# Kernel optimization log

Measured on AMD Instinct MI355X. Metric: run time of the kernel, lower is better.

The kernel has to match this reference:

```python
import math
import jax, jax.numpy as jnp
import numpy as np

B, L, H = 32, 1024, 128

def setup_inputs() -> dict:
    key = jax.random.key(0)
    k1, k2, k3, k4 = jax.random.split(key, 4)
    a = jax.random.normal(k1, (B, L, H), dtype=jnp.float32)
    b = jax.random.normal(k2, (B, L, H), dtype=jnp.float32)
    mask_a = jax.random.randint(k3, (B, L, 1), 0, 2, dtype=jnp.int32)
    mask_b = jax.random.randint(k4, (B, L, 1), 0, 2, dtype=jnp.int32)
    temperature = jnp.asarray(1.0 / math.sqrt(H), dtype=jnp.float32)
    return {"a": a, "b": b, "mask_a": mask_a, "mask_b": mask_b, "temperature": temperature}

def reference(a, b, mask_a, mask_b, temperature):
    # scores: [B, La, Lb]
    scores = jnp.einsum('bld,bmd->blm', a, b) * temperature
    # outer product of token validity masks -> pair mask [B, La, Lb]
    mask = jnp.einsum('blk,bmk->blm', mask_a.astype(jnp.float32), mask_b.astype(jnp.float32)) > 0
    scores = jnp.where(mask, scores, jnp.float32(-10000.0))
    attention_a = jax.nn.softmax(scores, axis=1)  # normalize over La (columns)
    attention_b = jax.nn.softmax(scores, axis=2)  # normalize over Lb (rows)
    feature_a = jnp.einsum('blm,bmd->bld', attention_b, b)
    feature_b = jnp.einsum('blm,bmd->bld', attention_a, a)  # valid since La == Lb
    return (feature_a, feature_b)
```

## Files before the change

kernel.cpp:

```cpp
#include <hip/hip_runtime.h>
#include <math.h>

#define BN 32
#define LL 1024
#define HH 128

typedef __attribute__((ext_vector_type(8))) short short8;
typedef __attribute__((ext_vector_type(4))) float f32x4;

static const size_t SZ_BF = (size_t)BN * LL * HH * 2;

__device__ __forceinline__ ushort f2bf(float x) {
  union { float f; unsigned u; } c; c.f = x;
  unsigned r = c.u + 0x7fffu + ((c.u >> 16) & 1u);
  return (ushort)(r >> 16);
}
__device__ __forceinline__ float bf2f(ushort h) {
  union { unsigned u; float f; } c; c.u = ((unsigned)h) << 16;
  return c.f;
}
__device__ __forceinline__ short8 ld8(const ushort* p) {
  return *(const short8*)p;
}

__global__ __launch_bounds__(256) void k_convert(
    const float* __restrict__ a, const float* __restrict__ b,
    const int* __restrict__ mask_b,
    ushort* __restrict__ abf, ushort* __restrict__ bbf,
    ushort* __restrict__ aT, ushort* __restrict__ bT,
    float* __restrict__ meanb, float* __restrict__ invmean) {
  int bb = blockIdx.y;
  int l0 = blockIdx.x * 64;
  int which = blockIdx.z;
  const float* src = which ? b : a;
  ushort* dst  = which ? bbf : abf;
  ushort* dstT = which ? bT : aT;
  float* dmean = which ? meanb : invmean;
  __shared__ __align__(16) ushort T[128][72];
  __shared__ float accS[128];
  __shared__ float wgt[64];
  int t = threadIdx.x;
  if (t < 128) accS[t] = 0.f;
  if (t < 64)
    wgt[t] = which ? 1.0f : ((mask_b[bb * LL + l0 + t] == 0) ? 1.0f : 0.0f);
  int lrow = t >> 5;
  int dcol = (t & 31) * 4;
#pragma unroll
  for (int p = 0; p < 8; ++p) {
    int l = p * 8 + lrow;
    float4 v = *(const float4*)&src[((size_t)bb * LL + l0 + l) * HH + dcol];
    ushort4 u;
    u.x = f2bf(v.x); u.y = f2bf(v.y); u.z = f2bf(v.z); u.w = f2bf(v.w);
    *(ushort4*)&dst[((size_t)bb * LL + l0 + l) * HH + dcol] = u;
    T[dcol + 0][l] = u.x; T[dcol + 1][l] = u.y;
    T[dcol + 2][l] = u.z; T[dcol + 3][l] = u.w;
  }
  __syncthreads();
  int drow = t >> 3;
  int c8 = (t & 7) * 8;
#pragma unroll
  for (int q = 0; q < 4; ++q) {
    int d = q * 32 + drow;
    short8 val = *(const short8*)&T[d][c8];
    *(short8*)&dstT[((size_t)bb * HH + d) * LL + l0 + c8] = val;
    float s = 0.f;
#pragma unroll
    for (int j = 0; j < 8; ++j) s += wgt[c8 + j] * bf2f((ushort)val[j]);
    atomicAdd(&accS[d], s);
  }
  __syncthreads();
  if (t < 128) atomicAdd(&dmean[bb * HH + t], accS[t]);
}


__global__ __launch_bounds__(256, 2) void k_colsum(
    const ushort* __restrict__ abf, const ushort* __restrict__ bbf,
    const int* __restrict__ mask_a, const int* __restrict__ mask_b,
    const float* __restrict__ temp_p, float2* __restrict__ cc) {
  int wg = blockIdx.x;
  int xcd = wg & 7, k_ = wg >> 3;
  int bb = (k_ >> 4) * 8 + xcd;
  int m0 = (k_ & 15) * 64;
  int t = threadIdx.x;
  int w = t >> 6, lane = t & 63, l16 = lane & 15, quad = lane >> 4;
  float temp = temp_p[0];
  __shared__ __align__(16) float biasA[LL];
  __shared__ float csred[4][4][16];
  for (int i = t; i < LL; i += 256)
    biasA[i] = mask_a[bb * LL + i] ? 0.0f : -10000.0f;

  short8 Bm[4][4];
  float biasB_mt[4];
#pragma unroll
  for (int mt = 0; mt < 4; ++mt) {
    int m = m0 + mt * 16 + l16;
    biasB_mt[mt] = mask_b[bb * LL + m] ? 0.0f : -10000.0f;
#pragma unroll
    for (int k = 0; k < 4; ++k)
      Bm[mt][k] = ld8(&bbf[((size_t)bb * LL + m) * HH + k * 32 + quad * 8]);
  }
  __syncthreads();

  float cs[4] = {0.f, 0.f, 0.f, 0.f};
  short8 Al0[4], Al1[4];

#define LOADAL(AlX, IT)                                                       \
  {                                                                           \
    const ushort* arow = &abf[((size_t)bb * LL + w * 256 + (IT) * 16 + l16) * HH]; \
    _Pragma("unroll") for (int k = 0; k < 4; ++k)                             \
        AlX[k] = ld8(&arow[k * 32 + quad * 8]);                               \
  }

#define CSCOMPUTE(AlX, IT)                                                    \
  {                                                                           \
    int lbase = w * 256 + (IT) * 16;                                          \
    f32x4 bA = *(const f32x4*)&biasA[lbase + quad * 4];                       \
    _Pragma("unroll") for (int mt = 0; mt < 4; ++mt) {                        \
      f32x4 sacc = {0.f, 0.f, 0.f, 0.f};                                      \
      _Pragma("unroll") for (int k = 0; k < 4; ++k)                           \
          sacc = __builtin_amdgcn_mfma_f32_16x16x32_bf16(AlX[k], Bm[mt][k],   \
                                                         sacc, 0, 0, 0);      \
      _Pragma("unroll") for (int r = 0; r < 4; ++r)                           \
          cs[mt] += __expf(sacc[r] * temp + bA[r] + biasB_mt[mt]);            \
    }                                                                         \
  }

  LOADAL(Al0, 0);
  for (int it = 0; it < 16; it += 2) {
    LOADAL(Al1, it + 1);
    CSCOMPUTE(Al0, it);
    LOADAL(Al0, (it + 2) & 15);
    CSCOMPUTE(Al1, it + 1);
  }
#undef LOADAL
#undef CSCOMPUTE

#pragma unroll
  for (int mt = 0; mt < 4; ++mt) {
    cs[mt] += __shfl_xor(cs[mt], 16);
    cs[mt] += __shfl_xor(cs[mt], 32);
  }
  if (lane < 16) {
#pragma unroll
    for (int mt = 0; mt < 4; ++mt) csred[w][mt][l16] = cs[mt];
  }
  __syncthreads();
  if (t < 64) {
    int mt = t >> 4, ml = t & 15;
    float s = csred[0][mt][ml] + csred[1][mt][ml] + csred[2][mt][ml] + csred[3][mt][ml];
    int m = m0 + t;
    float bB = mask_b[bb * LL + m] ? 0.0f : -10000.0f;
    cc[bb * LL + m] = make_float2(s > 0.f ? 1.0f / s : 0.0f, bB);
  }
}

__global__ __launch_bounds__(256, 2) void k_features(
    const ushort* __restrict__ abf, const ushort* __restrict__ bbf,
    const ushort* __restrict__ aT, const ushort* __restrict__ bT,
    const int* __restrict__ mask_a, const float* __restrict__ temp_p,
    const float2* __restrict__ cc, const float* __restrict__ meanb,
    const float* __restrict__ invmean, float* __restrict__ out) {
  int wg = blockIdx.x;
  int xcd = wg & 7, k_ = wg >> 3;
  int bb = (k_ >> 4) * 8 + xcd;
  int l0 = (k_ & 15) * 64;
  int t = threadIdx.x;
  int w = t >> 6, lane = t & 63, l16 = lane & 15, quad = lane >> 4;
  float temp = temp_p[0];

  __shared__ float2 ccs[LL];
  __shared__ __align__(16) ushort Pa[2][64 * 72];
  __shared__ __align__(16) ushort Pb[2][64 * 72];
  __shared__ float rspart[4][64];
  __shared__ float rsfin[64];

  for (int i = t; i < LL; i += 256) ccs[i] = cc[bb * LL + i];

  float biasA_lt[4];
  short8 Afix[4][4];
#pragma unroll
  for (int lt = 0; lt < 4; ++lt) {
    int l = l0 + lt * 16 + l16;
    biasA_lt[lt] = mask_a[bb * LL + l] ? 0.0f : -10000.0f;
#pragma unroll
    for (int k = 0; k < 4; ++k)
      Afix[lt][k] = ld8(&abf[((size_t)bb * LL + l) * HH + k * 32 + quad * 8]);
  }

  f32x4 accA[4][2], accB[4][2];
  f32x4 zero = {0.f, 0.f, 0.f, 0.f};
#pragma unroll
  for (int lt = 0; lt < 4; ++lt)
#pragma unroll
    for (int dt = 0; dt < 2; ++dt) { accA[lt][dt] = zero; accB[lt][dt] = zero; }
  float rs_lt[4] = {0.f, 0.f, 0.f, 0.f};
  __syncthreads();

  short8 Am0[4], Am1[4];
  float2 cv0[4], cv1[4];
  short8 Bb[2][2], Ba[2][2];

#define LOADAM(AmX, cvX, M0)                                                  \
  {                                                                           \
    const ushort* brow = &bbf[((size_t)bb * LL + (M0) + w * 16 + l16) * HH];  \
    _Pragma("unroll") for (int k = 0; k < 4; ++k)                             \
        AmX[k] = ld8(&brow[k * 32 + quad * 8]);                               \
    _Pragma("unroll") for (int r = 0; r < 4; ++r)                             \
        cvX[r] = ccs[(M0) + w * 16 + quad * 4 + r];                           \
  }

#define LOADBT(M0)                                                            \
  {                                                                           \
    _Pragma("unroll") for (int dt = 0; dt < 2; ++dt) {                        \
      const ushort* btrow =                                                   \
          &bT[((size_t)bb * HH + w * 32 + dt * 16 + l16) * LL + (M0)];        \
      const ushort* atrow =                                                   \
          &aT[((size_t)bb * HH + w * 32 + dt * 16 + l16) * LL + (M0)];        \
      _Pragma("unroll") for (int ks = 0; ks < 2; ++ks) {                      \
        Bb[dt][ks] = ld8(&btrow[ks * 32 + quad * 8]);                         \
        Ba[dt][ks] = ld8(&atrow[ks * 32 + quad * 8]);                         \
      }                                                                       \
    }                                                                         \
  }

#define SPHASE(AmX, cvX)                                                      \
  {                                                                           \
    ushort* pa = &Pa[buf][0];                                                 \
    ushort* pb = &Pb[buf][0];                                                 \
    _Pragma("unroll") for (int lt = 0; lt < 4; ++lt) {                        \
      f32x4 sacc = zero;                                                      \
      _Pragma("unroll") for (int k = 0; k < 4; ++k)                           \
          sacc = __builtin_amdgcn_mfma_f32_16x16x32_bf16(AmX[k], Afix[lt][k], \
                                                         sacc, 0, 0, 0);      \
      ushort pav[4], pbv[4];                                                  \
      _Pragma("unroll") for (int r = 0; r < 4; ++r) {                         \
        float e = __expf(sacc[r] * temp + biasA_lt[lt] + cvX[r].y);           \
        pav[r] = f2bf(e);                                                     \
        rs_lt[lt] += bf2f(pav[r]);                                            \
        pbv[r] = f2bf(e * cvX[r].x);                                          \
      }                                                                       \
      uint2 ka, kb;                                                           \
      ka.x = (uint)pav[0] | ((uint)pav[1] << 16);                             \
      ka.y = (uint)pav[2] | ((uint)pav[3] << 16);                             \
      kb.x = (uint)pbv[0] | ((uint)pbv[1] << 16);                             \
      kb.y = (uint)pbv[2] | ((uint)pbv[3] << 16);                             \
      int pidx = (lt * 16 + l16) * 72 + w * 16 + quad * 4;                    \
      *(uint2*)&pa[pidx] = ka;                                                \
      *(uint2*)&pb[pidx] = kb;                                                \
    }                                                                         \
  }

#define FPHASE()                                                              \
  {                                                                           \
    const ushort* pa = &Pa[buf][0];                                           \
    const ushort* pb = &Pb[buf][0];                                           \
    _Pragma("unroll") for (int lt = 0; lt < 4; ++lt) {                        \
      _Pragma("unroll") for (int ks = 0; ks < 2; ++ks) {                      \
        int ridx = (lt * 16 + l16) * 72 + ks * 32 + quad * 8;                 \
        short8 PaF = *(const short8*)&pa[ridx];                               \
        short8 PbF = *(const short8*)&pb[ridx];                               \
        _Pragma("unroll") for (int dt = 0; dt < 2; ++dt) {                    \
          accA[lt][dt] = __builtin_amdgcn_mfma_f32_16x16x32_bf16(             \
              PaF, Bb[dt][ks], accA[lt][dt], 0, 0, 0);                        \
          accB[lt][dt] = __builtin_amdgcn_mfma_f32_16x16x32_bf16(             \
              PbF, Ba[dt][ks], accB[lt][dt], 0, 0, 0);                        \
        }                                                                     \
      }                                                                       \
    }                                                                         \
  }

  LOADAM(Am0, cv0, 0);
  int buf = 0;
  for (int m0 = 0; m0 < LL; m0 += 128) {
    LOADBT(m0);
    LOADAM(Am1, cv1, m0 + 64);
    SPHASE(Am0, cv0);
    __syncthreads();
    FPHASE();
    buf ^= 1;
    LOADBT(m0 + 64);
    LOADAM(Am0, cv0, (m0 + 128) & (LL - 1));
    SPHASE(Am1, cv1);
    __syncthreads();
    FPHASE();
    buf ^= 1;
  }
#undef LOADAM
#undef LOADBT
#undef SPHASE
#undef FPHASE

#pragma unroll
  for (int lt = 0; lt < 4; ++lt) {
    rs_lt[lt] += __shfl_xor(rs_lt[lt], 16);
    rs_lt[lt] += __shfl_xor(rs_lt[lt], 32);
  }
  if (lane < 16) {
#pragma unroll
    for (int lt = 0; lt < 4; ++lt) rspart[w][lt * 16 + l16] = rs_lt[lt];
  }
  __syncthreads();
  if (t < 64)
    rsfin[t] = rspart[0][t] + rspart[1][t] + rspart[2][t] + rspart[3][t];
  __syncthreads();

  float* outA = out;
  float* outB = out + (size_t)BN * LL * HH;
#pragma unroll
  for (int dt = 0; dt < 2; ++dt) {
    int d = w * 32 + dt * 16 + l16;
    float mb = meanb[bb * HH + d] * (1.0f / 1024.0f);
    float im = invmean[bb * HH + d] * (1.0f / 1024.0f);
#pragma unroll
    for (int lt = 0; lt < 4; ++lt) {
#pragma unroll
      for (int r = 0; r < 4; ++r) {
        int l = lt * 16 + quad * 4 + r;
        float rsv = rsfin[l];
        float fa = (rsv > 0.f) ? accA[lt][dt][r] / rsv : mb;
        float fb = accB[lt][dt][r] + im;
        __builtin_nontemporal_store(fa, &outA[((size_t)bb * LL + l0 + l) * HH + d]);
        __builtin_nontemporal_store(fb, &outB[((size_t)bb * LL + l0 + l) * HH + d]);
      }
    }
  }
}

extern "C" void kernel_launch(void* const* d_in, const int* in_sizes, int n_in,
                              void* d_out, int out_size, void* d_ws, size_t ws_size,
                              hipStream_t stream) {
  const float* a = (const float*)d_in[0];
  const float* b = (const float*)d_in[1];
  const int* mask_a = (const int*)d_in[2];
  const int* mask_b = (const int*)d_in[3];
  const float* temp = (const float*)d_in[4];
  float* out = (float*)d_out;

  char* wsb = (char*)d_ws;
  ushort* abf = (ushort*)(wsb + 0 * SZ_BF);
  ushort* bbf = (ushort*)(wsb + 1 * SZ_BF);
  ushort* aT  = (ushort*)(wsb + 2 * SZ_BF);
  ushort* bT  = (ushort*)(wsb + 3 * SZ_BF);
  float2* cc  = (float2*)(wsb + 4 * SZ_BF);
  float* meanb   = (float*)(wsb + 4 * SZ_BF + (size_t)BN * LL * sizeof(float2));
  float* invmean = meanb + BN * HH;

  hipMemsetAsync(meanb, 0, 2 * BN * HH * sizeof(float), stream);
  k_convert<<<dim3(16, 32, 2), 256, 0, stream>>>(a, b, mask_b, abf, bbf, aT, bT,
                                                 meanb, invmean);
  k_colsum<<<dim3(512), 256, 0, stream>>>(abf, bbf, mask_a, mask_b, temp, cc);
  k_features<<<dim3(512), 256, 0, stream>>>(abf, bbf, aT, bT, mask_a, temp,
                                            cc, meanb, invmean, out);
  (void)in_sizes; (void)n_in; (void)out_size; (void)ws_size;
}
```

Measured before the change: 200.5 us.

## Software-pipeline the score phase of the next tile with the feature phase of the current tile

The main loop is restructured so that the score/exp phase for tile i+1 runs before the feature MFMA phase for tile i, with each writing or reading a different P buffer and one barrier per step. The B/A transposed tiles get double-buffered register sets, and a prologue and epilogue handle the pipeline fill and drain. The aim is to let exp/convert VALU work interleave with independent feature MFMAs and to hide global-load latency. The cost is extra VGPR pressure from the duplicated operand registers, which could lower occupancy or cause spills.

```diff
diff --git a/kernel.cpp b/kernel.cpp
--- a/kernel.cpp
+++ b/kernel.cpp
@@ -198,7 +198,7 @@
 
   short8 Am0[4], Am1[4];
   float2 cv0[4], cv1[4];
-  short8 Bb[2][2], Ba[2][2];
+  short8 Bb0[2][2], Ba0[2][2], Bb1[2][2], Ba1[2][2];
 
 #define LOADAM(AmX, cvX, M0)                                                  \
   {                                                                           \
@@ -209,7 +209,7 @@
         cvX[r] = ccs[(M0) + w * 16 + quad * 4 + r];                           \
   }
 
-#define LOADBT(M0)                                                            \
+#define LOADBT(BbX, BaX, M0)                                                  \
   {                                                                           \
     _Pragma("unroll") for (int dt = 0; dt < 2; ++dt) {                        \
       const ushort* btrow =                                                   \
@@ -217,16 +217,16 @@
       const ushort* atrow =                                                   \
           &aT[((size_t)bb * HH + w * 32 + dt * 16 + l16) * LL + (M0)];        \
       _Pragma("unroll") for (int ks = 0; ks < 2; ++ks) {                      \
-        Bb[dt][ks] = ld8(&btrow[ks * 32 + quad * 8]);                         \
-        Ba[dt][ks] = ld8(&atrow[ks * 32 + quad * 8]);                         \
+        BbX[dt][ks] = ld8(&btrow[ks * 32 + quad * 8]);                        \
+        BaX[dt][ks] = ld8(&atrow[ks * 32 + quad * 8]);                        \
       }                                                                       \
     }                                                                         \
   }
 
-#define SPHASE(AmX, cvX)                                                      \
-  {                                                                           \
-    ushort* pa = &Pa[buf][0];                                                 \
-    ushort* pb = &Pb[buf][0];                                                 \
+#define SPHASE(AmX, cvX, PBUFI)                                               \
+  {                                                                           \
+    ushort* pa = &Pa[PBUFI][0];                                               \
+    ushort* pb = &Pb[PBUFI][0];                                               \
     _Pragma("unroll") for (int lt = 0; lt < 4; ++lt) {                        \
       f32x4 sacc = zero;                                                      \
       _Pragma("unroll") for (int k = 0; k < 4; ++k)                           \
@@ -250,10 +250,10 @@
     }                                                                         \
   }
 
-#define FPHASE()                                                              \
-  {                                                                           \
-    const ushort* pa = &Pa[buf][0];                                           \
-    const ushort* pb = &Pb[buf][0];                                           \
+#define FPHASE(PBUFI, BbX, BaX)                                               \
+  {                                                                           \
+    const ushort* pa = &Pa[PBUFI][0];                                         \
+    const ushort* pb = &Pb[PBUFI][0];                                         \
     _Pragma("unroll") for (int lt = 0; lt < 4; ++lt) {                        \
       _Pragma("unroll") for (int ks = 0; ks < 2; ++ks) {                      \
         int ridx = (lt * 16 + l16) * 72 + ks * 32 + quad * 8;                 \
@@ -261,30 +261,40 @@
         short8 PbF = *(const short8*)&pb[ridx];                               \
         _Pragma("unroll") for (int dt = 0; dt < 2; ++dt) {                    \
           accA[lt][dt] = __builtin_amdgcn_mfma_f32_16x16x32_bf16(             \
-              PaF, Bb[dt][ks], accA[lt][dt], 0, 0, 0);                        \
+              PaF, BbX[dt][ks], accA[lt][dt], 0, 0, 0);                       \
           accB[lt][dt] = __builtin_amdgcn_mfma_f32_16x16x32_bf16(             \
-              PbF, Ba[dt][ks], accB[lt][dt], 0, 0, 0);                        \
+              PbF, BaX[dt][ks], accB[lt][dt], 0, 0, 0);                       \
         }                                                                     \
       }                                                                       \
     }                                                                         \
   }
 
   LOADAM(Am0, cv0, 0);
-  int buf = 0;
-  for (int m0 = 0; m0 < LL; m0 += 128) {
-    LOADBT(m0);
-    LOADAM(Am1, cv1, m0 + 64);
-    SPHASE(Am0, cv0);
+  LOADBT(Bb0, Ba0, 0);
+  LOADAM(Am1, cv1, 64);
+  SPHASE(Am0, cv0, 0);
+  __syncthreads();
+
+  for (int kk = 0; kk < 7; ++kk) {
+    int mA = (2 * kk + 1) * 64;
+    LOADBT(Bb1, Ba1, mA);
+    LOADAM(Am0, cv0, mA + 64);
+    SPHASE(Am1, cv1, 1);
+    FPHASE(0, Bb0, Ba0);
     __syncthreads();
-    FPHASE();
-    buf ^= 1;
-    LOADBT(m0 + 64);
-    LOADAM(Am0, cv0, (m0 + 128) & (LL - 1));
-    SPHASE(Am1, cv1);
+    LOADBT(Bb0, Ba0, mA + 64);
+    LOADAM(Am1, cv1, mA + 128);
+    SPHASE(Am0, cv0, 0);
+    FPHASE(1, Bb1, Ba1);
     __syncthreads();
-    FPHASE();
-    buf ^= 1;
-  }
+  }
+
+  LOADBT(Bb1, Ba1, 960);
+  SPHASE(Am1, cv1, 1);
+  FPHASE(0, Bb0, Ba0);
+  __syncthreads();
+  FPHASE(1, Bb1, Ba1);
+
 #undef LOADAM
 #undef LOADBT
 #undef SPHASE
```

New measurement: 200.7 us. About the same (+0.1%).
